# Performance work log

Hardware: AMD Instinct MI355X
Metric: run time of the kernel (lower is better)

The kernel has to match this reference:

```python
import jax, jax.numpy as jnp
import numpy as np

D_MODEL = 768
D_COND = 128
N_LAYERS = 6
D_STATE = 16
D_CONV = 4
EXPAND = 2
D_INNER = EXPAND * D_MODEL            # 1536
DT_RANK = (D_MODEL + 15) // 16        # 48
BATCH, SEQ = 2, 1024
EPS = 1e-5


def setup_inputs() -> dict:
    key = jax.random.key(0)
    ks = iter(jax.random.split(key, 24))
    rn = lambda shape, s=0.02: jax.random.normal(next(ks), shape, dtype=jnp.float32) * s
    inp = {}
    inp["x"] = jax.random.normal(next(ks), (BATCH, SEQ, D_MODEL), dtype=jnp.float32)
    inp["condition"] = jax.random.normal(next(ks), (BATCH, D_COND), dtype=jnp.float32)
    # per-layer Mamba params, stacked on leading layer dim
    inp["in_proj_w"] = rn((N_LAYERS, 2 * D_INNER, D_MODEL))
    inp["conv_w"] = rn((N_LAYERS, D_INNER, D_CONV), 0.1)
    inp["conv_b"] = jnp.zeros((N_LAYERS, D_INNER), jnp.float32)
    inp["x_proj_w"] = rn((N_LAYERS, DT_RANK + 2 * D_STATE, D_INNER))
    inp["dt_proj_w"] = rn((N_LAYERS, D_INNER, DT_RANK), 0.1)
    inp["dt_proj_b"] = jnp.full((N_LAYERS, D_INNER), -4.0, jnp.float32)  # softplus -> small dt
    inp["A_log"] = jnp.tile(jnp.log(jnp.arange(1, D_STATE + 1, dtype=jnp.float32))[None, None, :], (N_LAYERS, D_INNER, 1))
    inp["D_skip"] = jnp.ones((N_LAYERS, D_INNER), jnp.float32)
    inp["out_proj_w"] = rn((N_LAYERS, D_MODEL, D_INNER))
    # post-residual LayerNorm affine per layer
    inp["norm_w"] = jnp.ones((N_LAYERS, D_MODEL), jnp.float32)
    inp["norm_b"] = jnp.zeros((N_LAYERS, D_MODEL), jnp.float32)
    # AdaLN: condition -> (scale, shift)
    inp["adaln_w"] = rn((N_LAYERS, 2 * D_MODEL, D_COND))
    inp["adaln_b"] = jnp.zeros((N_LAYERS, 2 * D_MODEL), jnp.float32)
    inp["final_norm_w"] = jnp.ones((D_MODEL,), jnp.float32)
    inp["final_norm_b"] = jnp.zeros((D_MODEL,), jnp.float32)
    return inp


def _ln(h, w, b):
    mu = jnp.mean(h, -1, keepdims=True)
    var = jnp.mean(jnp.square(h - mu), -1, keepdims=True)
    return (h - mu) * jax.lax.rsqrt(var + EPS) * w + b


def _ln_noaffine(h):
    mu = jnp.mean(h, -1, keepdims=True)
    var = jnp.mean(jnp.square(h - mu), -1, keepdims=True)
    return (h - mu) * jax.lax.rsqrt(var + EPS)


def _mamba(x, in_w, cw, cb, xp_w, dtp_w, dtp_b, A_log, D_skip, out_w):
    b, l, _ = x.shape
    xz = jnp.einsum('bld,ed->ble', x, in_w)                 # [b,l,2*di]
    xc, z = jnp.split(xz, 2, axis=-1)
    # causal depthwise conv over time
    xc_t = jnp.transpose(xc, (0, 2, 1))                     # [b,di,l]
    xc_t = jax.lax.conv_general_dilated(
        xc_t, cw[:, None, :], window_strides=(1,), padding=[(D_CONV - 1, 0)],
        dimension_numbers=('NCH', 'OIH', 'NCH'), feature_group_count=D_INNER)
    xc = jnp.transpose(xc_t + cb[None, :, None], (0, 2, 1))  # [b,l,di]
    xc = jax.nn.silu(xc)
    dbc = jnp.einsum('bld,ed->ble', xc, xp_w)                # [b,l,dt_rank+2*ds]
    dt = dbc[..., :DT_RANK]
    Bm = dbc[..., DT_RANK:DT_RANK + D_STATE]                 # [b,l,ds]
    Cm = dbc[..., DT_RANK + D_STATE:]                        # [b,l,ds]
    dt = jax.nn.softplus(jnp.einsum('blr,dr->bld', dt, dtp_w) + dtp_b)  # [b,l,di]
    A = -jnp.exp(A_log)                                      # [di,ds]

    def step(h, ts):
        dt_t, B_t, C_t, x_t = ts                             # [b,di],[b,ds],[b,ds],[b,di]
        dA = jnp.exp(dt_t[:, :, None] * A)                   # [b,di,ds]
        h = dA * h + (dt_t * x_t)[:, :, None] * B_t[:, None, :]
        y = jnp.sum(h * C_t[:, None, :], axis=-1)            # [b,di]
        return h, y

    h0 = jnp.zeros((b, D_INNER, D_STATE), x.dtype)
    ts = (jnp.transpose(dt, (1, 0, 2)), jnp.transpose(Bm, (1, 0, 2)),
          jnp.transpose(Cm, (1, 0, 2)), jnp.transpose(xc, (1, 0, 2)))
    h_final, y = jax.lax.scan(step, h0, ts)
    y = jnp.transpose(y, (1, 0, 2)) + D_skip * xc            # [b,l,di]
    y = y * jax.nn.silu(z)
    out = jnp.einsum('bld,ed->ble', y, out_w)                # [b,l,dm]
    return out, h_final


def reference(x, condition, in_proj_w, conv_w, conv_b, x_proj_w, dt_proj_w, dt_proj_b,
              A_log, D_skip, out_proj_w, norm_w, norm_b, adaln_w, adaln_b,
              final_norm_w, final_norm_b):
    h = x
    states = []
    for i in range(N_LAYERS):
        residual = h
        m, st = _mamba(h, in_proj_w[i], conv_w[i], conv_b[i], x_proj_w[i],
                       dt_proj_w[i], dt_proj_b[i], A_log[i], D_skip[i], out_proj_w[i])
        h = _ln(residual + m, norm_w[i], norm_b[i])
        ss = condition @ adaln_w[i].T + adaln_b[i]            # [b,2*dm]
        scale, shift = jnp.split(ss, 2, axis=-1)
        h = _ln_noaffine(h) * (1.0 + scale[:, None, :]) + shift[:, None, :]
        states.append(st)
    h = _ln(h, final_norm_w, final_norm_b)
    return h, jnp.stack(states)
```

## Files before the change

### kernel.cpp

```cpp
#include <hip/hip_runtime.h>
#include <hip/hip_bf16.h>

#define NL 6
#define DM 768
#define DI 1536
#define DS 16
#define NRANK 48
#define DBC 80
#define BATCH 2
#define SEQ 1024
#define NTOK (BATCH*SEQ)
#define NCHUNK 64
#define CHLEN 16
#define XKS 8
#define XKC (DI/XKS)

typedef __attribute__((ext_vector_type(8))) short short8;
typedef __attribute__((ext_vector_type(4))) float f32x4;
typedef __attribute__((ext_vector_type(4))) unsigned short ushort4v;

__device__ inline unsigned short f2bf(float f) {
  union { float f; unsigned u; } x; x.f = f;
  unsigned r = x.u + 0x7FFF + ((x.u >> 16) & 1);
  return (unsigned short)(r >> 16);
}
__device__ inline float bf2f(unsigned short s) {
  union { unsigned u; float f; } x; x.u = ((unsigned)s) << 16;
  return x.f;
}

__device__ inline void gl_lds16(const unsigned short* g, unsigned short* l) {
  __builtin_amdgcn_global_load_lds(
      (const __attribute__((address_space(1))) unsigned int*)(g),
      (__attribute__((address_space(3))) unsigned int*)(l),
      16, 0, 0);
}

#define SPAN_X   (NTOK * DM / 4)
#define SPAN_INW (NL * 2 * DI * DM / 4)
#define SPAN_OUW (NL * DM * DI / 4)
#define SPAN_XPW (NL * DBC * DI / 4)
#define SPAN_ALL (SPAN_X + SPAN_INW + SPAN_OUW + SPAN_XPW)

__device__ inline void cvt4_store(const float* s, unsigned short* d, int i) {
  f32x4 v = ((const f32x4*)s)[i];
  union { ushort4v u4; __hip_bfloat162 h[2]; } u;
  float2 p;
  p.x = v[0]; p.y = v[1]; u.h[0] = __float22bfloat162_rn(p);
  p.x = v[2]; p.y = v[3]; u.h[1] = __float22bfloat162_rn(p);
  ((ushort4v*)d)[i] = u.u4;
}

__global__ __launch_bounds__(256) void cvtall_k(const float* __restrict__ x,
                                                const float* __restrict__ inw,
                                                const float* __restrict__ ouw,
                                                const float* __restrict__ xpw,
                                                unsigned short* __restrict__ xb,
                                                unsigned short* __restrict__ inwb,
                                                unsigned short* __restrict__ ouwb,
                                                unsigned short* __restrict__ xpwb,
                                                float* __restrict__ hc) {
  for (int i = blockIdx.x * 256 + threadIdx.x; i < SPAN_ALL; i += gridDim.x * 256) {
    if (i < SPAN_X) {
      f32x4 v = ((const f32x4*)x)[i];
      ((f32x4*)hc)[i] = v;
      union { ushort4v u4; __hip_bfloat162 h[2]; } u;
      float2 p;
      p.x = v[0]; p.y = v[1]; u.h[0] = __float22bfloat162_rn(p);
      p.x = v[2]; p.y = v[3]; u.h[1] = __float22bfloat162_rn(p);
      ((ushort4v*)xb)[i] = u.u4;
    }
    else if (i < SPAN_X + SPAN_INW) cvt4_store(inw, inwb, i - SPAN_X);
    else if (i < SPAN_X + SPAN_INW + SPAN_OUW) cvt4_store(ouw, ouwb, i - SPAN_X - SPAN_INW);
    else cvt4_store(xpw, xpwb, i - SPAN_X - SPAN_INW - SPAN_OUW);
  }
}

__global__ __launch_bounds__(256) void misc_pre_k(const float* __restrict__ w,
                                                  const float* __restrict__ al,
                                                  unsigned short* __restrict__ wb,
                                                  float* __restrict__ na) {
  int idx = blockIdx.x * 256 + threadIdx.x;
  const int NDT = NL * 1536 * 64;
  if (idx < NDT) {
    int col = idx & 63;
    int row = idx >> 6;
    wb[idx] = (col < NRANK) ? f2bf(w[(size_t)row * NRANK + col]) : (unsigned short)0;
  } else if (idx < NDT + NL * DI * DS) {
    int k = idx - NDT;
    na[k] = -__expf(al[k]);
  }
}

__global__ __launch_bounds__(256) void bt128b_k(
    const unsigned short* __restrict__ A, int lda,
    const unsigned short* __restrict__ W, int ldw,
    unsigned short* __restrict__ C, int ldc,
    int K) {
  __shared__ __align__(16) unsigned short As[2][128 * 32];
  __shared__ __align__(16) unsigned short Ws[2][128 * 32];
  const int tid = threadIdx.x;
  const int bm = blockIdx.y * 128;
  const int bn = blockIdx.x * 128;
  const int lane = tid & 63;
  const int wv = tid >> 6;
  const int wm = (wv >> 1) * 64;
  const int wn = (wv & 1) * 64;
  const int fr = lane & 15;
  const int fs = lane >> 4;

  const int r0 = tid >> 2;
  const int s0 = (tid & 3) ^ (r0 & 3);

  const unsigned short* gA0 = A + (size_t)(bm + r0) * lda + s0 * 8;
  const unsigned short* gA1 = A + (size_t)(bm + r0 + 64) * lda + s0 * 8;
  const unsigned short* gW0 = W + (size_t)(bn + r0) * ldw + s0 * 8;
  const unsigned short* gW1 = W + (size_t)(bn + r0 + 64) * ldw + s0 * 8;

  f32x4 acc[4][4];
#pragma unroll
  for (int i = 0; i < 4; i++)
#pragma unroll
    for (int j = 0; j < 4; j++) acc[i][j] = (f32x4){0.f, 0.f, 0.f, 0.f};

  gl_lds16(gA0, &As[0][0] + tid * 8);
  gl_lds16(gA1, &As[0][2048] + tid * 8);
  gl_lds16(gW0, &Ws[0][0] + tid * 8);
  gl_lds16(gW1, &Ws[0][2048] + tid * 8);
  __syncthreads();

  const int nk = K >> 5;
  int buf = 0;
  for (int kk = 0; kk < nk; kk++) {
    if (kk + 1 < nk) {
      const int k0 = (kk + 1) * 32;
      gl_lds16(gA0 + k0, &As[buf ^ 1][0] + tid * 8);
      gl_lds16(gA1 + k0, &As[buf ^ 1][2048] + tid * 8);
      gl_lds16(gW0 + k0, &Ws[buf ^ 1][0] + tid * 8);
      gl_lds16(gW1 + k0, &Ws[buf ^ 1][2048] + tid * 8);
    }

    short8 af[4], bf[4];
#pragma unroll
    for (int i = 0; i < 4; i++) {
      int rowa = wm + i * 16 + fr;
      af[i] = *(const short8*)&As[buf][rowa * 32 + ((fs ^ (rowa & 3)) * 8)];
      int rowb = wn + i * 16 + fr;
      bf[i] = *(const short8*)&Ws[buf][rowb * 32 + ((fs ^ (rowb & 3)) * 8)];
    }
#pragma unroll
    for (int i = 0; i < 4; i++)
#pragma unroll
      for (int j = 0; j < 4; j++)
        acc[i][j] = __builtin_amdgcn_mfma_f32_16x16x32_bf16(af[i], bf[j], acc[i][j], 0, 0, 0);

    __syncthreads();
    buf ^= 1;
  }

#pragma unroll
  for (int i = 0; i < 4; i++) {
#pragma unroll
    for (int j = 0; j < 4; j++) {
#pragma unroll
      for (int r = 0; r < 4; r++) {
        int row = bm + wm + i * 16 + fs * 4 + r;
        int col = bn + wn + j * 16 + fr;
        C[(size_t)row * ldc + col] = f2bf(acc[i][j][r]);
      }
    }
  }
}

template<int EPI>
__global__ __launch_bounds__(256) void bt64_k(
    const unsigned short* __restrict__ A, int lda,
    const unsigned short* __restrict__ W, int ldw,
    void* __restrict__ Cv, int ldc,
    int K,
    const float* __restrict__ bias,
    const float* __restrict__ resid) {
  __shared__ __align__(16) unsigned short As[2][64 * 32];
  __shared__ __align__(16) unsigned short Ws[2][64 * 32];
  const int tid = threadIdx.x;
  const int bm = blockIdx.y * 64;
  const int bn = blockIdx.x * 64;
  const int lane = tid & 63;
  const int wv = tid >> 6;
  const int wm = (wv >> 1) * 32;
  const int wn = (wv & 1) * 32;
  const int fr = lane & 15;
  const int fs = lane >> 4;

  const int r0 = tid >> 2;
  const int s0 = (tid & 3) ^ (r0 & 3);

  const unsigned short* gA = A + (size_t)(bm + r0) * lda + s0 * 8;
  const unsigned short* gW = W + (size_t)(bn + r0) * ldw + s0 * 8;

  f32x4 acc[2][2];
#pragma unroll
  for (int i = 0; i < 2; i++)
#pragma unroll
    for (int j = 0; j < 2; j++) acc[i][j] = (f32x4){0.f, 0.f, 0.f, 0.f};

  gl_lds16(gA, &As[0][0] + tid * 8);
  gl_lds16(gW, &Ws[0][0] + tid * 8);
  __syncthreads();

  const int nk = K >> 5;
  int buf = 0;
  for (int kk = 0; kk < nk; kk++) {
    if (kk + 1 < nk) {
      const int k0 = (kk + 1) * 32;
      gl_lds16(gA + k0, &As[buf ^ 1][0] + tid * 8);
      gl_lds16(gW + k0, &Ws[buf ^ 1][0] + tid * 8);
    }

    short8 af[2], bf[2];
#pragma unroll
    for (int i = 0; i < 2; i++) {
      int rowa = wm + i * 16 + fr;
      af[i] = *(const short8*)&As[buf][rowa * 32 + ((fs ^ (rowa & 3)) * 8)];
      int rowb = wn + i * 16 + fr;
      bf[i] = *(const short8*)&Ws[buf][rowb * 32 + ((fs ^ (rowb & 3)) * 8)];
    }
#pragma unroll
    for (int i = 0; i < 2; i++)
#pragma unroll
      for (int j = 0; j < 2; j++)
        acc[i][j] = __builtin_amdgcn_mfma_f32_16x16x32_bf16(af[i], bf[j], acc[i][j], 0, 0, 0);

    __syncthreads();
    buf ^= 1;
  }

#pragma unroll
  for (int i = 0; i < 2; i++) {
#pragma unroll
    for (int j = 0; j < 2; j++) {
#pragma unroll
      for (int r = 0; r < 4; r++) {
        int row = bm + wm + i * 16 + fs * 4 + r;
        int col = bn + wn + j * 16 + fr;
        float v = acc[i][j][r];
        if (EPI == 1) {
          float xv = v + bias[col];
          float sp = (xv > 20.f) ? xv : log1pf(__expf(xv));
          ((unsigned short*)Cv)[(size_t)row * ldc + col] = f2bf(sp);
        }
        if (EPI == 2) {
          ((float*)Cv)[(size_t)row * ldc + col] = v + resid[(size_t)row * ldc + col];
        }
      }
    }
  }
}

__global__ __launch_bounds__(256) void xp_k(
    const unsigned short* __restrict__ A,
    const unsigned short* __restrict__ W,
    float* __restrict__ part) {
  __shared__ __align__(16) unsigned short As[64][40];
  __shared__ __align__(16) unsigned short Ws[80][40];
  const int tid = threadIdx.x;
  const int ks = blockIdx.x;
  const int bm = blockIdx.y * 64;
  const int lane = tid & 63;
  const int wv = tid >> 6;
  const int fr = lane & 15;
  const int fs = lane >> 4;
  const int fk = fs * 8;

  const int ar = tid >> 2;
  const int ac = (tid & 3) * 8;
  const int k0base = ks * XKC;

  const unsigned short* gA  = A + (size_t)(bm + ar) * DI + k0base + ac;
  const unsigned short* gW0 = W + (size_t)ar * DI + k0base + ac;
  const unsigned short* gW1 = W + (size_t)(64 + ar) * DI + k0base + ac;

  f32x4 acc[5];
#pragma unroll
  for (int n = 0; n < 5; n++) acc[n] = (f32x4){0.f, 0.f, 0.f, 0.f};

  short8 aA, w0A, w1A;
  aA = *(const short8*)(gA);
  w0A = *(const short8*)(gW0);
  if (tid < 64) w1A = *(const short8*)(gW1);

  const int nk = XKC / 32;
  for (int kk = 0; kk < nk; kk++) {
    __syncthreads();
    *(short8*)&As[ar][ac] = aA;
    *(short8*)&Ws[ar][ac] = w0A;
    if (tid < 64) *(short8*)&Ws[64 + ar][ac] = w1A;
    __syncthreads();

    if (kk + 1 < nk) {
      const int k0 = (kk + 1) * 32;
      aA = *(const short8*)(gA + k0);
      w0A = *(const short8*)(gW0 + k0);
      if (tid < 64) w1A = *(const short8*)(gW1 + k0);
    }

    short8 af = *(const short8*)&As[wv * 16 + fr][fk];
#pragma unroll
    for (int n = 0; n < 5; n++) {
      short8 bf = *(const short8*)&Ws[n * 16 + fr][fk];
      acc[n] = __builtin_amdgcn_mfma_f32_16x16x32_bf16(af, bf, acc[n], 0, 0, 0);
    }
  }

#pragma unroll
  for (int n = 0; n < 5; n++) {
#pragma unroll
    for (int r = 0; r < 4; r++) {
      int row = bm + wv * 16 + fs * 4 + r;
      part[((size_t)ks * NTOK + row) * DBC + n * 16 + fr] = acc[n][r];
    }
  }
}

__global__ __launch_bounds__(256) void xp_reduce_k(const float* __restrict__ part,
                                                   float* __restrict__ dbc,
                                                   unsigned short* __restrict__ dtA) {
  int i = blockIdx.x * 256 + threadIdx.x;
  const f32x4* p4 = (const f32x4*)part;
  const int stride4 = NTOK * DBC / 4;
  f32x4 s = p4[i];
#pragma unroll
  for (int ks = 1; ks < XKS; ks++) {
    f32x4 v = p4[(size_t)ks * stride4 + i];
    s[0] += v[0]; s[1] += v[1]; s[2] += v[2]; s[3] += v[3];
  }
  ((f32x4*)dbc)[i] = s;
  int c4 = (i * 4) % DBC;
  int m = (i * 4) / DBC;
  if (c4 < 64) {
    union { ushort4v u4; __hip_bfloat162 h[2]; } u;
    if (c4 < NRANK) {
      float2 p;
      p.x = s[0]; p.y = s[1]; u.h[0] = __float22bfloat162_rn(p);
      p.x = s[2]; p.y = s[3]; u.h[1] = __float22bfloat162_rn(p);
    } else {
      u.u4 = (ushort4v){0, 0, 0, 0};
    }
    *(ushort4v*)&dtA[(size_t)m * 64 + c4] = u.u4;
  }
}

__global__ __launch_bounds__(256) void conv_silu_k(const unsigned short* __restrict__ xz,
                                                   const float* __restrict__ cw,
                                                   const float* __restrict__ cb,
                                                   unsigned short* __restrict__ xcb) {
  const int d = blockIdx.x * 256 + threadIdx.x;
  const int l0 = blockIdx.y * 16;
  const int b = blockIdx.z;
  const size_t mbase = (size_t)b * SEQ;
  const float w0 = cw[d * 4 + 0], w1 = cw[d * 4 + 1];
  const float w2 = cw[d * 4 + 2], w3 = cw[d * 4 + 3];
  const float bias = cb[d];
  float c3 = (l0 >= 3) ? bf2f(xz[(mbase + l0 - 3) * (2 * DI) + d]) : 0.f;
  float c2 = (l0 >= 2) ? bf2f(xz[(mbase + l0 - 2) * (2 * DI) + d]) : 0.f;
  float c1 = (l0 >= 1) ? bf2f(xz[(mbase + l0 - 1) * (2 * DI) + d]) : 0.f;
#pragma unroll
  for (int t = 0; t < 16; t++) {
    const int l = l0 + t;
    float cur = bf2f(xz[(mbase + l) * (2 * DI) + d]);
    float s = bias + w0 * c3 + w1 * c2 + w2 * c1 + w3 * cur;
    float sig = 1.f / (1.f + __expf(-s));
    xcb[(mbase + l) * DI + d] = f2bf(s * sig);
    c3 = c2; c2 = c1; c1 = cur;
  }
}

__global__ __launch_bounds__(256) void scan1_k(const unsigned short* __restrict__ dt,
                                               const unsigned short* __restrict__ xc,
                                               const float* __restrict__ dbc,
                                               const float* __restrict__ negA_l,
                                               unsigned int* __restrict__ ch_pk,
                                               unsigned short* __restrict__ yloc,
                                               float* __restrict__ cumdt) {
  __shared__ float Bs[CHLEN][DS];
  __shared__ float Cs[CHLEN][DS];
  const int tid = threadIdx.x;
  const int j = blockIdx.x;
  const int cg = blockIdx.y;
  const int b = cg / 6;
  const int d = (cg % 6) * 256 + tid;
  const int c = b * DI + d;
  const int m0 = b * SEQ + j * CHLEN;

  for (int e = tid; e < CHLEN * 32; e += 256) {
    int row = e >> 5, col = e & 31;
    float v = dbc[(size_t)(m0 + row) * DBC + NRANK + col];
    if (col < DS) Bs[row][col] = v; else Cs[row][col - DS] = v;
  }

  float Av[DS];
  const float* na = negA_l + (size_t)d * DS;
#pragma unroll
  for (int s = 0; s < DS; s++) Av[s] = na[s];
  const float Av0 = Av[0];
  bool fast = true;
#pragma unroll
  for (int s = 0; s < DS; s++)
    fast = fast && (fabsf(Av[s] - (s + 1) * Av0) <= 1e-4f * (s + 1));

  float dts[CHLEN], xcs[CHLEN];
#pragma unroll
  for (int t = 0; t < CHLEN; t++) {
    dts[t] = bf2f(dt[(size_t)(m0 + t) * DI + d]);
    xcs[t] = bf2f(xc[(size_t)(m0 + t) * DI + d]);
  }
  __syncthreads();

  float h[DS];
#pragma unroll
  for (int s = 0; s < DS; s++) h[s] = 0.f;
  float cd = 0.f;

  for (int t = 0; t < CHLEN; t++) {
    float dtv = dts[t];
    cd += dtv;
    float dtx = dtv * xcs[t];
    float ysum = 0.f;
    if (fast) {
      float e1 = __expf(dtv * Av0);
      float dA = e1;
      h[0] = fmaf(dA, h[0], dtx * Bs[t][0]);
      ysum = fmaf(h[0], Cs[t][0], ysum);
#pragma unroll
      for (int s = 1; s < DS; s++) {
        dA *= e1;
        h[s] = fmaf(dA, h[s], dtx * Bs[t][s]);
        ysum = fmaf(h[s], Cs[t][s], ysum);
      }
    } else {
#pragma unroll
      for (int s = 0; s < DS; s++) {
        float dA = __expf(dtv * Av[s]);
        h[s] = fmaf(dA, h[s], dtx * Bs[t][s]);
        ysum = fmaf(h[s], Cs[t][s], ysum);
      }
    }
    size_t mi = (size_t)(m0 + t) * DI + d;
    yloc[mi] = f2bf(ysum);
    cumdt[mi] = cd;
  }

  size_t base = ((size_t)j * (BATCH * DI) + c) * DS;
#pragma unroll
  for (int s = 0; s < DS; s++) {
    unsigned int pk = (unsigned int)f2bf(__expf(cd * Av[s]))
                    | ((unsigned int)f2bf(h[s]) << 16);
    ch_pk[base + s] = pk;
  }
}

__global__ __launch_bounds__(256) void scan2_k(const unsigned int* __restrict__ ch_pk,
                                               unsigned short* __restrict__ hin,
                                               float* __restrict__ states_out) {
  int idx = blockIdx.x * 256 + threadIdx.x;
  const int stride = BATCH * DI * DS;
  float h = 0.f;
  for (int j = 0; j < NCHUNK; j++) {
    hin[(size_t)j * stride + idx] = f2bf(h);
    unsigned int pk = ch_pk[(size_t)j * stride + idx];
    float ca = bf2f((unsigned short)(pk & 0xFFFF));
    float hl = bf2f((unsigned short)(pk >> 16));
    h = fmaf(ca, h, hl);
  }
  states_out[idx] = h;
}

__global__ __launch_bounds__(256) void scanfix_k(const unsigned short* __restrict__ yloc,
                                                 const float* __restrict__ cumdt,
                                                 const unsigned short* __restrict__ xc,
                                                 const unsigned short* __restrict__ xz,
                                                 const float* __restrict__ dbc,
                                                 const float* __restrict__ negA_l,
                                                 const float* __restrict__ Dsk,
                                                 const unsigned short* __restrict__ hin,
                                                 unsigned short* __restrict__ y) {
  int idx = blockIdx.x * 256 + threadIdx.x;
  int d = idx % DI;
  int m = idx / DI;
  int b = m / SEQ;
  int j = (m % SEQ) / CHLEN;
  float cd = cumdt[idx];
  float yv = bf2f(yloc[idx]);
  const f32x4* na4 = (const f32x4*)(negA_l + (size_t)d * DS);
  const f32x4* cp4 = (const f32x4*)(dbc + (size_t)m * DBC + NRANK + DS);
  const ushort4v* h4 = (const ushort4v*)(hin + ((size_t)j * (BATCH * DI) + (size_t)b * DI + d) * DS);
  float corr = 0.f;
#pragma unroll
  for (int q = 0; q < 4; q++) {
    f32x4 na = na4[q], cp = cp4[q];
    ushort4v hh = h4[q];
#pragma unroll
    for (int e = 0; e < 4; e++)
      corr = fmaf(__expf(cd * na[e]) * bf2f(hh[e]), cp[e], corr);
  }
  yv += corr;
  float xv = bf2f(xc[idx]);
  float zv = bf2f(xz[(size_t)m * (2 * DI) + DI + d]);
  float sig = 1.f / (1.f + __expf(-zv));
  y[idx] = f2bf((yv + Dsk[d] * xv) * (zv * sig));
}

template<bool ADA>
__global__ __launch_bounds__(256) void ln_k(const float* __restrict__ in,
                                            const float* __restrict__ w,
                                            const float* __restrict__ bb,
                                            const float* __restrict__ ss,
                                            float* __restrict__ out,
                                            unsigned short* __restrict__ outb) {
  __shared__ float red[8];
  const int row = blockIdx.x;
  const int bt = row / SEQ;
  const int tid = threadIdx.x;
  const float* x = in + (size_t)row * DM;
  float v[3];
#pragma unroll
  for (int i = 0; i < 3; i++) v[i] = x[tid + i * 256];
  float s1 = v[0] + v[1] + v[2];
  float s2 = v[0]*v[0] + v[1]*v[1] + v[2]*v[2];
#pragma unroll
  for (int o = 32; o > 0; o >>= 1) { s1 += __shfl_down(s1, o); s2 += __shfl_down(s2, o); }
  int wv = tid >> 6, ln = tid & 63;
  if (ln == 0) { red[wv*2] = s1; red[wv*2+1] = s2; }
  __syncthreads();
  s1 = red[0] + red[2] + red[4] + red[6];
  s2 = red[1] + red[3] + red[5] + red[7];
  float mu = s1 * (1.f / DM);
  float var = s2 * (1.f / DM) - mu * mu;
  float rs = rsqrtf(var + 1e-5f);
  float t[3];
#pragma unroll
  for (int i = 0; i < 3; i++) {
    int c = tid + i * 256;
    t[i] = (v[i] - mu) * rs * w[c] + bb[c];
  }
  if (!ADA) {
#pragma unroll
    for (int i = 0; i < 3; i++) out[(size_t)row * DM + tid + i * 256] = t[i];
    return;
  }
  __syncthreads();
  s1 = t[0] + t[1] + t[2];
  s2 = t[0]*t[0] + t[1]*t[1] + t[2]*t[2];
#pragma unroll
  for (int o = 32; o > 0; o >>= 1) { s1 += __shfl_down(s1, o); s2 += __shfl_down(s2, o); }
  if (ln == 0) { red[wv*2] = s1; red[wv*2+1] = s2; }
  __syncthreads();
  s1 = red[0] + red[2] + red[4] + red[6];
  s2 = red[1] + red[3] + red[5] + red[7];
  float mu2 = s1 * (1.f / DM);
  float var2 = s2 * (1.f / DM) - mu2 * mu2;
  float rs2 = rsqrtf(var2 + 1e-5f);
#pragma unroll
  for (int i = 0; i < 3; i++) {
    int c = tid + i * 256;
    float sc = ss[bt * (2 * DM) + c];
    float sh = ss[bt * (2 * DM) + DM + c];
    float r = (t[i] - mu2) * rs2 * (1.f + sc) + sh;
    out[(size_t)row * DM + c] = r;
    outb[(size_t)row * DM + c] = f2bf(r);
  }
}

__global__ __launch_bounds__(256) void adaln_pre_k(const float* __restrict__ cond,
                                                   const float* __restrict__ aw,
                                                   const float* __restrict__ ab,
                                                   float* __restrict__ ss) {
  int idx = blockIdx.x * 256 + threadIdx.x;
  int e = idx % (2 * DM);
  int b = (idx / (2 * DM)) % BATCH;
  int l = idx / (BATCH * 2 * DM);
  const float* c = cond + b * 128;
  const float* wp = aw + ((size_t)l * (2 * DM) + e) * 128;
  float s = ab[l * (2 * DM) + e];
  for (int k = 0; k < 128; k++) s = fmaf(c[k], wp[k], s);
  ss[idx] = s;
}

extern "C" void kernel_launch(void* const* d_in, const int* in_sizes, int n_in,
                              void* d_out, int out_size, void* d_ws, size_t ws_size,
                              hipStream_t stream) {
  const float* x      = (const float*)d_in[0];
  const float* cond   = (const float*)d_in[1];
  const float* in_w   = (const float*)d_in[2];
  const float* conv_w = (const float*)d_in[3];
  const float* conv_b = (const float*)d_in[4];
  const float* xp_w   = (const float*)d_in[5];
  const float* dtp_w  = (const float*)d_in[6];
  const float* dtp_b  = (const float*)d_in[7];
  const float* A_log  = (const float*)d_in[8];
  const float* Dsk    = (const float*)d_in[9];
  const float* out_w  = (const float*)d_in[10];
  const float* norm_w = (const float*)d_in[11];
  const float* norm_b = (const float*)d_in[12];
  const float* ada_w  = (const float*)d_in[13];
  const float* ada_b  = (const float*)d_in[14];
  const float* fn_w   = (const float*)d_in[15];
  const float* fn_b   = (const float*)d_in[16];

  float* out_h = (float*)d_out;
  float* out_states = out_h + (size_t)NTOK * DM;

  float* p = (float*)d_ws;
  float* h_cur = p; p += (size_t)NTOK * DM;
  float* dbc   = p; p += (size_t)NTOK * DBC;
  float* res2  = p; p += (size_t)NTOK * DM;
  float* ss    = p; p += (size_t)NL * BATCH * 2 * DM;
  float* xpart = p; p += (size_t)XKS * NTOK * DBC;
  float* negA  = p; p += (size_t)NL * DI * DS;
  float* cumdt = p; p += (size_t)NTOK * DI;
  unsigned int* ch_pk = (unsigned int*)p; p += (size_t)NCHUNK * BATCH * DI * DS;
  unsigned short* q = (unsigned short*)p;
  unsigned short* hin      = q; q += (size_t)NCHUNK * BATCH * DI * DS;
  unsigned short* in_w_bf  = q; q += (size_t)NL * 2 * DI * DM;
  unsigned short* out_w_bf = q; q += (size_t)NL * DM * DI;
  unsigned short* xp_w_bf  = q; q += (size_t)NL * DBC * DI;
  unsigned short* dtw_bf   = q; q += (size_t)NL * DI * 64;
  unsigned short* h_bf     = q; q += (size_t)NTOK * DM;
  unsigned short* xz_bf    = q; q += (size_t)NTOK * 2 * DI;
  unsigned short* xc_bf    = q; q += (size_t)NTOK * DI;
  unsigned short* dtb_bf   = q; q += (size_t)NTOK * DI;
  unsigned short* yb_bf    = q; q += (size_t)NTOK * DI;
  unsigned short* yloc_bf  = q; q += (size_t)NTOK * DI;
  unsigned short* dtA_bf   = q; q += (size_t)NTOK * 64;

  adaln_pre_k<<<72, 256, 0, stream>>>(cond, ada_w, ada_b, ss);
  cvtall_k<<<2048, 256, 0, stream>>>(x, in_w, out_w, xp_w,
                                     h_bf, in_w_bf, out_w_bf, xp_w_bf, h_cur);
  misc_pre_k<<<(NL * 1536 * 64 + NL * DI * DS + 255) / 256, 256, 0, stream>>>(
      dtp_w, A_log, dtw_bf, negA);

  for (int l = 0; l < NL; l++) {
    bt128b_k<<<dim3(24, 16), 256, 0, stream>>>(
        h_bf, DM, in_w_bf + (size_t)l * 2 * DI * DM, DM, xz_bf, 2 * DI, DM);
    conv_silu_k<<<dim3(DI / 256, SEQ / 16, BATCH), 256, 0, stream>>>(
        xz_bf, conv_w + (size_t)l * DI * 4, conv_b + (size_t)l * DI, xc_bf);
    xp_k<<<dim3(XKS, NTOK / 64), 256, 0, stream>>>(
        xc_bf, xp_w_bf + (size_t)l * DBC * DI, xpart);
    xp_reduce_k<<<NTOK * DBC / 4 / 256, 256, 0, stream>>>(xpart, dbc, dtA_bf);
    bt64_k<1><<<dim3(DI / 64, NTOK / 64), 256, 0, stream>>>(
        dtA_bf, 64, dtw_bf + (size_t)l * DI * 64, 64, dtb_bf, DI,
        64, dtp_b + (size_t)l * DI, nullptr);
    scan1_k<<<dim3(NCHUNK, 12), 256, 0, stream>>>(
        dtb_bf, xc_bf, dbc, negA + (size_t)l * DI * DS, ch_pk, yloc_bf, cumdt);
    scan2_k<<<192, 256, 0, stream>>>(
        ch_pk, hin, out_states + (size_t)l * BATCH * DI * DS);
    scanfix_k<<<NTOK * DI / 256, 256, 0, stream>>>(
        yloc_bf, cumdt, xc_bf, xz_bf, dbc, negA + (size_t)l * DI * DS,
        Dsk + (size_t)l * DI, hin, yb_bf);
    bt64_k<2><<<dim3(DM / 64, NTOK / 64), 256, 0, stream>>>(
        yb_bf, DI, out_w_bf + (size_t)l * DM * DI, DI, res2, DM,
        DI, nullptr, h_cur);
    ln_k<true><<<NTOK, 256, 0, stream>>>(
        res2, norm_w + (size_t)l * DM, norm_b + (size_t)l * DM,
        ss + (size_t)l * BATCH * 2 * DM, h_cur, h_bf);
  }
  ln_k<false><<<NTOK, 256, 0, stream>>>(h_cur, fn_w, fn_b, nullptr, out_h, nullptr);
}
```

Before: 786.9 us.

## Merge setup kernels, store scan intermediates in bf16, vectorize conv

Folds the three preprocessing kernels (weight conversion, dt/A prep, AdaLN scale/shift) into one grid-stride setup kernel. The x_proj split-K partials, the reduced B/C values and the scan's local y and cumulative dt are now kept in bf16, with y and cumulative dt packed into one 32-bit word, which cuts the traffic between xp, reduce, scan1 and scanfix. The conv+SiLU kernel now handles two channels per thread with paired loads and stores. The price is extra bf16 rounding on partial sums and on cumulative dt, which feeds an exponent, so accuracy may suffer.

```diff
diff --git a/kernel.cpp b/kernel.cpp
--- a/kernel.cpp
+++ b/kernel.cpp
@@ -36,11 +36,15 @@
       16, 0, 0);
 }
 
-#define SPAN_X   (NTOK * DM / 4)
-#define SPAN_INW (NL * 2 * DI * DM / 4)
-#define SPAN_OUW (NL * DM * DI / 4)
-#define SPAN_XPW (NL * DBC * DI / 4)
-#define SPAN_ALL (SPAN_X + SPAN_INW + SPAN_OUW + SPAN_XPW)
+#define U_X   (NTOK * DM / 4)
+#define U_INW (NL * 2 * DI * DM / 4)
+#define U_OUW (NL * DM * DI / 4)
+#define U_XPW (NL * DBC * DI / 4)
+#define U_DTW (NL * DI * 64 / 4)
+#define U_NA  (NL * DI * DS / 4)
+#define U_DTA (NTOK * 64 / 4)
+#define U_ADA (NL * BATCH * 2 * DM)
+#define U_ALL (U_X + U_INW + U_OUW + U_XPW + U_DTW + U_NA + U_DTA + U_ADA)
 
 __device__ inline void cvt4_store(const float* s, unsigned short* d, int i) {
   f32x4 v = ((const f32x4*)s)[i];
@@ -51,44 +55,75 @@
   ((ushort4v*)d)[i] = u.u4;
 }
 
-__global__ __launch_bounds__(256) void cvtall_k(const float* __restrict__ x,
-                                                const float* __restrict__ inw,
-                                                const float* __restrict__ ouw,
-                                                const float* __restrict__ xpw,
-                                                unsigned short* __restrict__ xb,
-                                                unsigned short* __restrict__ inwb,
-                                                unsigned short* __restrict__ ouwb,
-                                                unsigned short* __restrict__ xpwb,
-                                                float* __restrict__ hc) {
-  for (int i = blockIdx.x * 256 + threadIdx.x; i < SPAN_ALL; i += gridDim.x * 256) {
-    if (i < SPAN_X) {
-      f32x4 v = ((const f32x4*)x)[i];
-      ((f32x4*)hc)[i] = v;
+__global__ __launch_bounds__(256) void setup_k(
+    const float* __restrict__ x, const float* __restrict__ inw,
+    const float* __restrict__ ouw, const float* __restrict__ xpw,
+    const float* __restrict__ dtpw, const float* __restrict__ alog,
+    const float* __restrict__ cond, const float* __restrict__ adaw,
+    const float* __restrict__ adab,
+    unsigned short* __restrict__ xb, unsigned short* __restrict__ inwb,
+    unsigned short* __restrict__ ouwb, unsigned short* __restrict__ xpwb,
+    unsigned short* __restrict__ dtwb, float* __restrict__ na,
+    unsigned short* __restrict__ dtA, float* __restrict__ ss,
+    float* __restrict__ hc) {
+  for (int i = blockIdx.x * 256 + threadIdx.x; i < U_ALL; i += gridDim.x * 256) {
+    int k = i;
+    if (k < U_X) {
+      f32x4 v = ((const f32x4*)x)[k];
+      ((f32x4*)hc)[k] = v;
       union { ushort4v u4; __hip_bfloat162 h[2]; } u;
       float2 p;
       p.x = v[0]; p.y = v[1]; u.h[0] = __float22bfloat162_rn(p);
       p.x = v[2]; p.y = v[3]; u.h[1] = __float22bfloat162_rn(p);
-      ((ushort4v*)xb)[i] = u.u4;
-    }
-    else if (i < SPAN_X + SPAN_INW) cvt4_store(inw, inwb, i - SPAN_X);
-    else if (i < SPAN_X + SPAN_INW + SPAN_OUW) cvt4_store(ouw, ouwb, i - SPAN_X - SPAN_INW);
-    else cvt4_store(xpw, xpwb, i - SPAN_X - SPAN_INW - SPAN_OUW);
-  }
-}
-
-__global__ __launch_bounds__(256) void misc_pre_k(const float* __restrict__ w,
-                                                  const float* __restrict__ al,
-                                                  unsigned short* __restrict__ wb,
-                                                  float* __restrict__ na) {
-  int idx = blockIdx.x * 256 + threadIdx.x;
-  const int NDT = NL * 1536 * 64;
-  if (idx < NDT) {
-    int col = idx & 63;
-    int row = idx >> 6;
-    wb[idx] = (col < NRANK) ? f2bf(w[(size_t)row * NRANK + col]) : (unsigned short)0;
-  } else if (idx < NDT + NL * DI * DS) {
-    int k = idx - NDT;
-    na[k] = -__expf(al[k]);
+      ((ushort4v*)xb)[k] = u.u4;
+      continue;
+    }
+    k -= U_X;
+    if (k < U_INW) { cvt4_store(inw, inwb, k); continue; }
+    k -= U_INW;
+    if (k < U_OUW) { cvt4_store(ouw, ouwb, k); continue; }
+    k -= U_OUW;
+    if (k < U_XPW) { cvt4_store(xpw, xpwb, k); continue; }
+    k -= U_XPW;
+    if (k < U_DTW) {
+      int col4 = (k & 15) * 4;
+      int row = k >> 4;
+      ushort4v u4;
+      if (col4 < NRANK) {
+        const float* src = dtpw + (size_t)row * NRANK + col4;
+        u4[0] = f2bf(src[0]); u4[1] = f2bf(src[1]);
+        u4[2] = f2bf(src[2]); u4[3] = f2bf(src[3]);
+      } else {
+        u4 = (ushort4v){0, 0, 0, 0};
+      }
+      *(ushort4v*)&dtwb[(size_t)row * 64 + col4] = u4;
+      continue;
+    }
+    k -= U_DTW;
+    if (k < U_NA) {
+      f32x4 v = ((const f32x4*)alog)[k];
+      f32x4 r;
+#pragma unroll
+      for (int e = 0; e < 4; e++) r[e] = -__expf(v[e]);
+      ((f32x4*)na)[k] = r;
+      continue;
+    }
+    k -= U_NA;
+    if (k < U_DTA) {
+      ((ushort4v*)dtA)[k] = (ushort4v){0, 0, 0, 0};
+      continue;
+    }
+    k -= U_DTA;
+    {
+      int e = k % (2 * DM);
+      int b = (k / (2 * DM)) % BATCH;
+      int l = k / (BATCH * 2 * DM);
+      const float* c = cond + b * 128;
+      const float* wp = adaw + ((size_t)l * (2 * DM) + e) * 128;
+      float s = adab[l * (2 * DM) + e];
+      for (int kk = 0; kk < 128; kk++) s = fmaf(c[kk], wp[kk], s);
+      ss[k] = s;
+    }
   }
 }
 
@@ -260,7 +295,7 @@
 __global__ __launch_bounds__(256) void xp_k(
     const unsigned short* __restrict__ A,
     const unsigned short* __restrict__ W,
-    float* __restrict__ part) {
+    unsigned short* __restrict__ part) {
   __shared__ __align__(16) unsigned short As[64][40];
   __shared__ __align__(16) unsigned short Ws[80][40];
   const int tid = threadIdx.x;
@@ -317,36 +352,31 @@
 #pragma unroll
     for (int r = 0; r < 4; r++) {
       int row = bm + wv * 16 + fs * 4 + r;
-      part[((size_t)ks * NTOK + row) * DBC + n * 16 + fr] = acc[n][r];
-    }
-  }
-}
-
-__global__ __launch_bounds__(256) void xp_reduce_k(const float* __restrict__ part,
-                                                   float* __restrict__ dbc,
-                                                   unsigned short* __restrict__ dtA) {
+      part[((size_t)ks * NTOK + row) * DBC + n * 16 + fr] = f2bf(acc[n][r]);
+    }
+  }
+}
+
+__global__ __launch_bounds__(256) void xp_reduce_k(const unsigned short* __restrict__ part,
+                                                   unsigned short* __restrict__ dtA,
+                                                   unsigned short* __restrict__ bc) {
   int i = blockIdx.x * 256 + threadIdx.x;
-  const f32x4* p4 = (const f32x4*)part;
+  const ushort4v* p4 = (const ushort4v*)part;
   const int stride4 = NTOK * DBC / 4;
-  f32x4 s = p4[i];
-#pragma unroll
-  for (int ks = 1; ks < XKS; ks++) {
-    f32x4 v = p4[(size_t)ks * stride4 + i];
-    s[0] += v[0]; s[1] += v[1]; s[2] += v[2]; s[3] += v[3];
-  }
-  ((f32x4*)dbc)[i] = s;
+  float s0 = 0.f, s1 = 0.f, s2 = 0.f, s3 = 0.f;
+#pragma unroll
+  for (int ks = 0; ks < XKS; ks++) {
+    ushort4v v = p4[(size_t)ks * stride4 + i];
+    s0 += bf2f(v[0]); s1 += bf2f(v[1]); s2 += bf2f(v[2]); s3 += bf2f(v[3]);
+  }
+  ushort4v o;
+  o[0] = f2bf(s0); o[1] = f2bf(s1); o[2] = f2bf(s2); o[3] = f2bf(s3);
   int c4 = (i * 4) % DBC;
   int m = (i * 4) / DBC;
-  if (c4 < 64) {
-    union { ushort4v u4; __hip_bfloat162 h[2]; } u;
-    if (c4 < NRANK) {
-      float2 p;
-      p.x = s[0]; p.y = s[1]; u.h[0] = __float22bfloat162_rn(p);
-      p.x = s[2]; p.y = s[3]; u.h[1] = __float22bfloat162_rn(p);
-    } else {
-      u.u4 = (ushort4v){0, 0, 0, 0};
-    }
-    *(ushort4v*)&dtA[(size_t)m * 64 + c4] = u.u4;
+  if (c4 < NRANK) {
+    *(ushort4v*)&dtA[(size_t)m * 64 + c4] = o;
+  } else {
+    *(ushort4v*)&bc[(size_t)m * 32 + (c4 - NRANK)] = o;
   }
 }
 
@@ -354,34 +384,42 @@
                                                    const float* __restrict__ cw,
                                                    const float* __restrict__ cb,
                                                    unsigned short* __restrict__ xcb) {
-  const int d = blockIdx.x * 256 + threadIdx.x;
+  const int d0 = (blockIdx.x * 256 + threadIdx.x) * 2;
   const int l0 = blockIdx.y * 16;
   const int b = blockIdx.z;
   const size_t mbase = (size_t)b * SEQ;
-  const float w0 = cw[d * 4 + 0], w1 = cw[d * 4 + 1];
-  const float w2 = cw[d * 4 + 2], w3 = cw[d * 4 + 3];
-  const float bias = cb[d];
-  float c3 = (l0 >= 3) ? bf2f(xz[(mbase + l0 - 3) * (2 * DI) + d]) : 0.f;
-  float c2 = (l0 >= 2) ? bf2f(xz[(mbase + l0 - 2) * (2 * DI) + d]) : 0.f;
-  float c1 = (l0 >= 1) ? bf2f(xz[(mbase + l0 - 1) * (2 * DI) + d]) : 0.f;
+  const float wa0 = cw[d0 * 4 + 0], wa1 = cw[d0 * 4 + 1];
+  const float wa2 = cw[d0 * 4 + 2], wa3 = cw[d0 * 4 + 3];
+  const float wb0 = cw[d0 * 4 + 4], wb1 = cw[d0 * 4 + 5];
+  const float wb2 = cw[d0 * 4 + 6], wb3 = cw[d0 * 4 + 7];
+  const float ba = cb[d0], bb = cb[d0 + 1];
+
+  float a3 = 0.f, a2 = 0.f, a1 = 0.f, b3 = 0.f, b2 = 0.f, b1 = 0.f;
+  if (l0 >= 3) { ushort2 u = *(const ushort2*)&xz[(mbase + l0 - 3) * (2 * DI) + d0]; a3 = bf2f(u.x); b3 = bf2f(u.y); }
+  if (l0 >= 2) { ushort2 u = *(const ushort2*)&xz[(mbase + l0 - 2) * (2 * DI) + d0]; a2 = bf2f(u.x); b2 = bf2f(u.y); }
+  if (l0 >= 1) { ushort2 u = *(const ushort2*)&xz[(mbase + l0 - 1) * (2 * DI) + d0]; a1 = bf2f(u.x); b1 = bf2f(u.y); }
 #pragma unroll
   for (int t = 0; t < 16; t++) {
     const int l = l0 + t;
-    float cur = bf2f(xz[(mbase + l) * (2 * DI) + d]);
-    float s = bias + w0 * c3 + w1 * c2 + w2 * c1 + w3 * cur;
-    float sig = 1.f / (1.f + __expf(-s));
-    xcb[(mbase + l) * DI + d] = f2bf(s * sig);
-    c3 = c2; c2 = c1; c1 = cur;
+    ushort2 u = *(const ushort2*)&xz[(mbase + l) * (2 * DI) + d0];
+    float ca = bf2f(u.x), cbv = bf2f(u.y);
+    float sa = ba + wa0 * a3 + wa1 * a2 + wa2 * a1 + wa3 * ca;
+    float sb = bb + wb0 * b3 + wb1 * b2 + wb2 * b1 + wb3 * cbv;
+    float ra = sa / (1.f + __expf(-sa));
+    float rb = sb / (1.f + __expf(-sb));
+    ushort2 o; o.x = f2bf(ra); o.y = f2bf(rb);
+    *(ushort2*)&xcb[(mbase + l) * DI + d0] = o;
+    a3 = a2; a2 = a1; a1 = ca;
+    b3 = b2; b2 = b1; b1 = cbv;
   }
 }
 
 __global__ __launch_bounds__(256) void scan1_k(const unsigned short* __restrict__ dt,
                                                const unsigned short* __restrict__ xc,
-                                               const float* __restrict__ dbc,
+                                               const unsigned short* __restrict__ bc,
                                                const float* __restrict__ negA_l,
                                                unsigned int* __restrict__ ch_pk,
-                                               unsigned short* __restrict__ yloc,
-                                               float* __restrict__ cumdt) {
+                                               unsigned int* __restrict__ yc_pk) {
   __shared__ float Bs[CHLEN][DS];
   __shared__ float Cs[CHLEN][DS];
   const int tid = threadIdx.x;
@@ -394,7 +432,7 @@
 
   for (int e = tid; e < CHLEN * 32; e += 256) {
     int row = e >> 5, col = e & 31;
-    float v = dbc[(size_t)(m0 + row) * DBC + NRANK + col];
+    float v = bf2f(bc[(size_t)(m0 + row) * 32 + col]);
     if (col < DS) Bs[row][col] = v; else Cs[row][col - DS] = v;
   }
 
@@ -445,9 +483,8 @@
         ysum = fmaf(h[s], Cs[t][s], ysum);
       }
     }
-    size_t mi = (size_t)(m0 + t) * DI + d;
-    yloc[mi] = f2bf(ysum);
-    cumdt[mi] = cd;
+    yc_pk[(size_t)(m0 + t) * DI + d] =
+        (unsigned int)f2bf(ysum) | ((unsigned int)f2bf(cd) << 16);
   }
 
   size_t base = ((size_t)j * (BATCH * DI) + c) * DS;
@@ -475,11 +512,10 @@
   states_out[idx] = h;
 }
 
-__global__ __launch_bounds__(256) void scanfix_k(const unsigned short* __restrict__ yloc,
-                                                 const float* __restrict__ cumdt,
+__global__ __launch_bounds__(256) void scanfix_k(const unsigned int* __restrict__ yc_pk,
                                                  const unsigned short* __restrict__ xc,
                                                  const unsigned short* __restrict__ xz,
-                                                 const float* __restrict__ dbc,
+                                                 const unsigned short* __restrict__ bc,
                                                  const float* __restrict__ negA_l,
                                                  const float* __restrict__ Dsk,
                                                  const unsigned short* __restrict__ hin,
@@ -489,19 +525,21 @@
   int m = idx / DI;
   int b = m / SEQ;
   int j = (m % SEQ) / CHLEN;
-  float cd = cumdt[idx];
-  float yv = bf2f(yloc[idx]);
+  unsigned int pk = yc_pk[idx];
+  float yv = bf2f((unsigned short)(pk & 0xFFFF));
+  float cd = bf2f((unsigned short)(pk >> 16));
   const f32x4* na4 = (const f32x4*)(negA_l + (size_t)d * DS);
-  const f32x4* cp4 = (const f32x4*)(dbc + (size_t)m * DBC + NRANK + DS);
+  const ushort4v* cp4 = (const ushort4v*)(bc + (size_t)m * 32 + DS);
   const ushort4v* h4 = (const ushort4v*)(hin + ((size_t)j * (BATCH * DI) + (size_t)b * DI + d) * DS);
   float corr = 0.f;
 #pragma unroll
   for (int q = 0; q < 4; q++) {
-    f32x4 na = na4[q], cp = cp4[q];
+    f32x4 na = na4[q];
+    ushort4v cp = cp4[q];
     ushort4v hh = h4[q];
 #pragma unroll
     for (int e = 0; e < 4; e++)
-      corr = fmaf(__expf(cd * na[e]) * bf2f(hh[e]), cp[e], corr);
+      corr = fmaf(__expf(cd * na[e]) * bf2f(hh[e]), bf2f(cp[e]), corr);
   }
   yv += corr;
   float xv = bf2f(xc[idx]);
@@ -569,21 +607,6 @@
     out[(size_t)row * DM + c] = r;
     outb[(size_t)row * DM + c] = f2bf(r);
   }
-}
-
-__global__ __launch_bounds__(256) void adaln_pre_k(const float* __restrict__ cond,
-                                                   const float* __restrict__ aw,
-                                                   const float* __restrict__ ab,
-                                                   float* __restrict__ ss) {
-  int idx = blockIdx.x * 256 + threadIdx.x;
-  int e = idx % (2 * DM);
-  int b = (idx / (2 * DM)) % BATCH;
-  int l = idx / (BATCH * 2 * DM);
-  const float* c = cond + b * 128;
-  const float* wp = aw + ((size_t)l * (2 * DM) + e) * 128;
-  float s = ab[l * (2 * DM) + e];
-  for (int k = 0; k < 128; k++) s = fmaf(c[k], wp[k], s);
-  ss[idx] = s;
 }
 
 extern "C" void kernel_launch(void* const* d_in, const int* in_sizes, int n_in,
@@ -612,13 +635,11 @@
 
   float* p = (float*)d_ws;
   float* h_cur = p; p += (size_t)NTOK * DM;
-  float* dbc   = p; p += (size_t)NTOK * DBC;
   float* res2  = p; p += (size_t)NTOK * DM;
   float* ss    = p; p += (size_t)NL * BATCH * 2 * DM;
-  float* xpart = p; p += (size_t)XKS * NTOK * DBC;
   float* negA  = p; p += (size_t)NL * DI * DS;
-  float* cumdt = p; p += (size_t)NTOK * DI;
   unsigned int* ch_pk = (unsigned int*)p; p += (size_t)NCHUNK * BATCH * DI * DS;
+  unsigned int* yc_pk = (unsigned int*)p; p += (size_t)NTOK * DI;
   unsigned short* q = (unsigned short*)p;
   unsigned short* hin      = q; q += (size_t)NCHUNK * BATCH * DI * DS;
   unsigned short* in_w_bf  = q; q += (size_t)NL * 2 * DI * DM;
@@ -630,32 +651,32 @@
   unsigned short* xc_bf    = q; q += (size_t)NTOK * DI;
   unsigned short* dtb_bf   = q; q += (size_t)NTOK * DI;
   unsigned short* yb_bf    = q; q += (size_t)NTOK * DI;
-  unsigned short* yloc_bf  = q; q += (size_t)NTOK * DI;
+  unsigned short* part_bf  = q; q += (size_t)XKS * NTOK * DBC;
   unsigned short* dtA_bf   = q; q += (size_t)NTOK * 64;
-
-  adaln_pre_k<<<72, 256, 0, stream>>>(cond, ada_w, ada_b, ss);
-  cvtall_k<<<2048, 256, 0, stream>>>(x, in_w, out_w, xp_w,
-                                     h_bf, in_w_bf, out_w_bf, xp_w_bf, h_cur);
-  misc_pre_k<<<(NL * 1536 * 64 + NL * DI * DS + 255) / 256, 256, 0, stream>>>(
-      dtp_w, A_log, dtw_bf, negA);
+  unsigned short* bc_bf    = q; q += (size_t)NTOK * 32;
+
+  setup_k<<<2048, 256, 0, stream>>>(x, in_w, out_w, xp_w, dtp_w, A_log,
+                                    cond, ada_w, ada_b,
+                                    h_bf, in_w_bf, out_w_bf, xp_w_bf, dtw_bf,
+                                    negA, dtA_bf, ss, h_cur);
 
   for (int l = 0; l < NL; l++) {
     bt128b_k<<<dim3(24, 16), 256, 0, stream>>>(
         h_bf, DM, in_w_bf + (size_t)l * 2 * DI * DM, DM, xz_bf, 2 * DI, DM);
-    conv_silu_k<<<dim3(DI / 256, SEQ / 16, BATCH), 256, 0, stream>>>(
+    conv_silu_k<<<dim3(DI / 512, SEQ / 16, BATCH), 256, 0, stream>>>(
         xz_bf, conv_w + (size_t)l * DI * 4, conv_b + (size_t)l * DI, xc_bf);
     xp_k<<<dim3(XKS, NTOK / 64), 256, 0, stream>>>(
-        xc_bf, xp_w_bf + (size_t)l * DBC * DI, xpart);
-    xp_reduce_k<<<NTOK * DBC / 4 / 256, 256, 0, stream>>>(xpart, dbc, dtA_bf);
+        xc_bf, xp_w_bf + (size_t)l * DBC * DI, part_bf);
+    xp_reduce_k<<<NTOK * DBC / 4 / 256, 256, 0, stream>>>(part_bf, dtA_bf, bc_bf);
     bt64_k<1><<<dim3(DI / 64, NTOK / 64), 256, 0, stream>>>(
         dtA_bf, 64, dtw_bf + (size_t)l * DI * 64, 64, dtb_bf, DI,
         64, dtp_b + (size_t)l * DI, nullptr);
     scan1_k<<<dim3(NCHUNK, 12), 256, 0, stream>>>(
-        dtb_bf, xc_bf, dbc, negA + (size_t)l * DI * DS, ch_pk, yloc_bf, cumdt);
+        dtb_bf, xc_bf, bc_bf, negA + (size_t)l * DI * DS, ch_pk, yc_pk);
     scan2_k<<<192, 256, 0, stream>>>(
         ch_pk, hin, out_states + (size_t)l * BATCH * DI * DS);
     scanfix_k<<<NTOK * DI / 256, 256, 0, stream>>>(
-        yloc_bf, cumdt, xc_bf, xz_bf, dbc, negA + (size_t)l * DI * DS,
+        yc_pk, xc_bf, xz_bf, bc_bf, negA + (size_t)l * DI * DS,
         Dsk + (size_t)l * DI, hin, yb_bf);
     bt64_k<2><<<dim3(DM / 64, NTOK / 64), 256, 0, stream>>>(
         yb_bf, DI, out_w_bf + (size_t)l * DM * DI, DI, res2, DM,
```

Measured after the change: 754.9 us. 1.04x faster.
